# Performance work log

Hardware: AMD Instinct MI355X
Metric: run time of the kernel (lower is better)

Reference implementation:

```python
import jax, jax.numpy as jnp
import numpy as np
from jax import lax

ITER = 10
SMOOTH = 1.0


def _max_pool3(x):
    # 3x3 max pool, stride 1, pad 1 (torch pads with -inf for max pool)
    return lax.reduce_window(x, -np.inf, lax.max,
                             window_dimensions=(1, 1, 3, 3),
                             window_strides=(1, 1, 1, 1),
                             padding=((0, 0), (0, 0), (1, 1), (1, 1)))


def soft_skeletonize(x, thresh_width=ITER):
    def body(i, x):
        min_pool_x = -_max_pool3(-x)
        contour = jax.nn.relu(_max_pool3(min_pool_x) - min_pool_x)
        return jax.nn.relu(x - contour)
    return lax.fori_loop(0, thresh_width, body, x)


def setup_inputs() -> dict:
    key = jax.random.key(0)
    k1, k2 = jax.random.split(key)
    shape = (32, 2, 512, 512)
    y_pred = jax.random.uniform(k1, shape, dtype=jnp.float32)
    y_true = jax.random.uniform(k2, shape, dtype=jnp.float32)
    return {"y_pred": y_pred, "y_true": y_true}


def reference(y_pred, y_true):
    skel_pred = soft_skeletonize(y_pred, ITER)
    skel_true = soft_skeletonize(y_true, ITER)
    tprec = (jnp.sum((skel_pred * y_true)[:, 1:]) + SMOOTH) / (jnp.sum(skel_pred[:, 1:]) + SMOOTH)
    tsens = (jnp.sum((skel_true * y_pred)[:, 1:]) + SMOOTH) / (jnp.sum(skel_true[:, 1:]) + SMOOTH)
    cl_dice = 1.0 - 2.0 * (tprec * tsens) / (tprec + tsens)
    return cl_dice
```

## Files before the change

### kernel.cpp

```cpp
#include <hip/hip_runtime.h>

#define IMG 512
#define HW (IMG * IMG)
#define NB 32
#define NIMG 64
#define BAND 32
#define NBAND (IMG / BAND)
#define NSTG 5
#define HALO (2 * NSTG)
#define NROWS (BAND + 2 * HALO)
#define INF __builtin_inff()

struct Row { float4 a, b; };

static __device__ __forceinline__ float min3f(float a, float b, float c) { return fminf(fminf(a, b), c); }
static __device__ __forceinline__ float max3f(float a, float b, float c) { return fmaxf(fmaxf(a, b), c); }

static __device__ __forceinline__ Row splat(float v) {
    Row r;
    r.a = make_float4(v, v, v, v);
    r.b = make_float4(v, v, v, v);
    return r;
}

static __device__ __forceinline__ Row rmin3(const Row& x, const Row& y, const Row& z) {
    Row o;
    const float* px = (const float*)&x;
    const float* py = (const float*)&y;
    const float* pz = (const float*)&z;
    float* po = (float*)&o;
#pragma unroll
    for (int i = 0; i < 8; ++i) po[i] = min3f(px[i], py[i], pz[i]);
    return o;
}

static __device__ __forceinline__ Row rmax3(const Row& x, const Row& y, const Row& z) {
    Row o;
    const float* px = (const float*)&x;
    const float* py = (const float*)&y;
    const float* pz = (const float*)&z;
    float* po = (float*)&o;
#pragma unroll
    for (int i = 0; i < 8; ++i) po[i] = max3f(px[i], py[i], pz[i]);
    return o;
}

static __device__ __forceinline__ Row hmin3(const Row& v, int lane) {
    float shl = __shfl_up(v.b.w, 1);
    float shr = __shfl_down(v.a.x, 1);
    if (lane == 0) shl = INF;
    if (lane == 63) shr = INF;
    Row o;
    o.a.x = min3f(shl,   v.a.x, v.a.y);
    o.a.y = min3f(v.a.x, v.a.y, v.a.z);
    o.a.z = min3f(v.a.y, v.a.z, v.a.w);
    o.a.w = min3f(v.a.z, v.a.w, v.b.x);
    o.b.x = min3f(v.a.w, v.b.x, v.b.y);
    o.b.y = min3f(v.b.x, v.b.y, v.b.z);
    o.b.z = min3f(v.b.y, v.b.z, v.b.w);
    o.b.w = min3f(v.b.z, v.b.w, shr);
    return o;
}

static __device__ __forceinline__ Row hmax3(const Row& v, int lane) {
    float shl = __shfl_up(v.b.w, 1);
    float shr = __shfl_down(v.a.x, 1);
    if (lane == 0) shl = -INF;
    if (lane == 63) shr = -INF;
    Row o;
    o.a.x = max3f(shl,   v.a.x, v.a.y);
    o.a.y = max3f(v.a.x, v.a.y, v.a.z);
    o.a.z = max3f(v.a.y, v.a.z, v.a.w);
    o.a.w = max3f(v.a.z, v.a.w, v.b.x);
    o.b.x = max3f(v.a.w, v.b.x, v.b.y);
    o.b.y = max3f(v.b.x, v.b.y, v.b.z);
    o.b.z = max3f(v.b.y, v.b.z, v.b.w);
    o.b.w = max3f(v.b.z, v.b.w, shr);
    return o;
}

template <int P>
static __device__ __forceinline__ Row stage_step(Row (&x)[2], Row (&mn)[2],
                                                 const Row& xin, int t, int lane) {
    Row vmin = rmin3(x[P], x[P ^ 1], xin);
    Row mnew = hmin3(vmin, lane);
    if ((unsigned)(t - 1) >= IMG) mnew = splat(-INF);
    Row vmax = rmax3(mn[P], mn[P ^ 1], mnew);
    Row mp = hmax3(vmax, lane);
    Row out;
    {
        const float* pxc = (const float*)&x[P];
        const float* pmn = (const float*)&mn[P ^ 1];
        const float* pmp = (const float*)&mp;
        float* po = (float*)&out;
#pragma unroll
        for (int i = 0; i < 8; ++i)
            po[i] = fmaxf(pxc[i] - fmaxf(pmp[i] - pmn[i], 0.f), 0.f);
    }
    if ((unsigned)(t - 2) >= IMG) out = splat(INF);
    x[P] = xin;
    mn[P] = mnew;
    return out;
}

static __device__ __forceinline__ Row load_or_inf(const float* __restrict__ p, int r, int lane) {
    if ((unsigned)r >= IMG) return splat(INF);
    const float4* q = (const float4*)(p + (size_t)r * IMG + lane * 8);
    Row o;
    o.a = q[0];
    o.b = q[1];
    return o;
}

template <int P>
static __device__ __forceinline__ void phase_a(int r, Row (&pre)[2], Row (&x)[NSTG][2],
                                               Row (&mn)[NSTG][2], const float* __restrict__ src,
                                               float* __restrict__ dst, int B, int lane) {
    Row cur = pre[P];
    pre[P] = load_or_inf(src, r + 2, lane);
    cur = stage_step<P>(x[0], mn[0], cur, r, lane);
    cur = stage_step<P>(x[1], mn[1], cur, r - 2, lane);
    cur = stage_step<P>(x[2], mn[2], cur, r - 4, lane);
    cur = stage_step<P>(x[3], mn[3], cur, r - 6, lane);
    cur = stage_step<P>(x[4], mn[4], cur, r - 8, lane);
    const int v = r - HALO;
    if ((unsigned)(v - B) < BAND) {
        float4* q = (float4*)(dst + (size_t)v * IMG + lane * 8);
        q[0] = cur.a;
        q[1] = cur.b;
    }
}

__global__ __launch_bounds__(64, 1) void skel5_a(const float* __restrict__ yp,
                                                 const float* __restrict__ yt,
                                                 float* __restrict__ mid) {
    const int blk = blockIdx.x;
    const int img = blk >> 4, band = blk & (NBAND - 1);
    const float* src = (img < NB) ? yp + (size_t)(2 * img + 1) * HW
                                  : yt + (size_t)(2 * (img - NB) + 1) * HW;
    float* dst = mid + (size_t)img * HW;
    const int lane = threadIdx.x;
    const int B = band * BAND;

    Row x[NSTG][2], mn[NSTG][2];
#pragma unroll
    for (int j = 0; j < NSTG; ++j) {
        x[j][0] = splat(INF);  x[j][1] = splat(INF);
        mn[j][0] = splat(-INF); mn[j][1] = splat(-INF);
    }
    Row pre[2];
    pre[0] = load_or_inf(src, B - HALO, lane);
    pre[1] = load_or_inf(src, B - HALO + 1, lane);

#pragma unroll 1
    for (int rr = 0; rr < NROWS; rr += 2) {
        phase_a<0>(B - HALO + rr, pre, x, mn, src, dst, B, lane);
        phase_a<1>(B - HALO + rr + 1, pre, x, mn, src, dst, B, lane);
    }
}

template <int P>
static __device__ __forceinline__ void phase_b(int r, Row (&pre)[2], Row (&wbuf)[2],
                                               Row (&x)[NSTG][2], Row (&mn)[NSTG][2],
                                               const float* __restrict__ src,
                                               const float* __restrict__ wp, int B, int lane,
                                               float& s_prod, float& s_val) {
    Row cur = pre[P];
    pre[P] = load_or_inf(src, r + 2, lane);
    cur = stage_step<P>(x[0], mn[0], cur, r, lane);
    cur = stage_step<P>(x[1], mn[1], cur, r - 2, lane);
    cur = stage_step<P>(x[2], mn[2], cur, r - 4, lane);
    cur = stage_step<P>(x[3], mn[3], cur, r - 6, lane);
    cur = stage_step<P>(x[4], mn[4], cur, r - 8, lane);
    const int v = r - HALO;
    if ((unsigned)(v - B) < BAND) {
        const Row w = wbuf[P];
        const float* pc = (const float*)&cur;
        const float* pw = (const float*)&w;
#pragma unroll
        for (int i = 0; i < 8; ++i) {
            s_prod += pc[i] * pw[i];
            s_val += pc[i];
        }
    }
    const int vn = r + 2 - HALO;
    if ((unsigned)(vn - B) < BAND) {
        const float4* q = (const float4*)(wp + (size_t)vn * IMG + lane * 8);
        wbuf[P].a = q[0];
        wbuf[P].b = q[1];
    }
}

__global__ __launch_bounds__(64, 1) void skel5_b(const float* __restrict__ mid,
                                                 const float* __restrict__ yp,
                                                 const float* __restrict__ yt,
                                                 double* __restrict__ acc) {
    const int blk = blockIdx.x;
    const int img = blk >> 4, band = blk & (NBAND - 1);
    const float* src = mid + (size_t)img * HW;
    const float* wp = (img < NB) ? yt + (size_t)(2 * img + 1) * HW
                                 : yp + (size_t)(2 * (img - NB) + 1) * HW;
    const int lane = threadIdx.x;
    const int B = band * BAND;

    Row x[NSTG][2], mn[NSTG][2];
#pragma unroll
    for (int j = 0; j < NSTG; ++j) {
        x[j][0] = splat(INF);  x[j][1] = splat(INF);
        mn[j][0] = splat(-INF); mn[j][1] = splat(-INF);
    }
    Row pre[2], wbuf[2];
    pre[0] = load_or_inf(src, B - HALO, lane);
    pre[1] = load_or_inf(src, B - HALO + 1, lane);
    wbuf[0] = splat(0.f);
    wbuf[1] = splat(0.f);

    float s_prod = 0.f, s_val = 0.f;
#pragma unroll 1
    for (int rr = 0; rr < NROWS; rr += 2) {
        phase_b<0>(B - HALO + rr, pre, wbuf, x, mn, src, wp, B, lane, s_prod, s_val);
        phase_b<1>(B - HALO + rr + 1, pre, wbuf, x, mn, src, wp, B, lane, s_prod, s_val);
    }
#pragma unroll
    for (int off = 32; off; off >>= 1) {
        s_prod += __shfl_down(s_prod, off);
        s_val += __shfl_down(s_val, off);
    }
    if (lane == 0) {
        const int base = (img < NB) ? 0 : 2;
        atomicAdd(&acc[base], (double)s_prod);
        atomicAdd(&acc[base + 1], (double)s_val);
    }
}

__global__ void finalize(const double* __restrict__ acc, float* __restrict__ out) {
    double tprec = (acc[0] + 1.0) / (acc[1] + 1.0);
    double tsens = (acc[2] + 1.0) / (acc[3] + 1.0);
    out[0] = (float)(1.0 - 2.0 * (tprec * tsens) / (tprec + tsens));
}

extern "C" void kernel_launch(void* const* d_in, const int* in_sizes, int n_in,
                              void* d_out, int out_size, void* d_ws, size_t ws_size,
                              hipStream_t stream) {
    (void)in_sizes; (void)n_in; (void)out_size; (void)ws_size;
    const float* yp = (const float*)d_in[0];
    const float* yt = (const float*)d_in[1];
    float* out = (float*)d_out;

    float* mid = (float*)d_ws;
    double* acc = (double*)(mid + (size_t)NIMG * HW);

    hipMemsetAsync(acc, 0, 4 * sizeof(double), stream);

    const int grid = NIMG * NBAND;
    skel5_a<<<grid, 64, 0, stream>>>(yp, yt, mid);
    skel5_b<<<grid, 64, 0, stream>>>(mid, yp, yt, acc);
    finalize<<<1, 1, 0, stream>>>(acc, out);
}
```

Baseline: 275.6 us.

## Halve band height, process two rows per step, specialize edge bands

Halving the band height doubles the number of blocks, so each SIMD has more independent waves to hide latency. The pipeline step now advances two rows at once to expose more instruction-level parallelism. A template flag removes the image-boundary checks for interior bands. The cost is that the fixed halo becomes a larger share of each band, so more rows are recomputed redundantly, and the wider step raises register pressure under the new launch bound of two blocks.

```diff
diff --git a/kernel.cpp b/kernel.cpp
--- a/kernel.cpp
+++ b/kernel.cpp
@@ -4,11 +4,11 @@
 #define HW (IMG * IMG)
 #define NB 32
 #define NIMG 64
-#define BAND 32
+#define BAND 16
 #define NBAND (IMG / BAND)
 #define NSTG 5
 #define HALO (2 * NSTG)
-#define NROWS (BAND + 2 * HALO)
+#define NSTEP ((BAND + 2 * HALO) / 2)
 #define INF __builtin_inff()
 
 struct Row { float4 a, b; };
@@ -79,28 +79,44 @@
     return o;
 }
 
-template <int P>
-static __device__ __forceinline__ Row stage_step(Row (&x)[2], Row (&mn)[2],
-                                                 const Row& xin, int t, int lane) {
-    Row vmin = rmin3(x[P], x[P ^ 1], xin);
-    Row mnew = hmin3(vmin, lane);
-    if ((unsigned)(t - 1) >= IMG) mnew = splat(-INF);
-    Row vmax = rmax3(mn[P], mn[P ^ 1], mnew);
-    Row mp = hmax3(vmax, lane);
-    Row out;
+template <bool EDGE>
+static __device__ __forceinline__ void step2(Row (&x)[2], Row (&mn)[2],
+                                             Row& in0, Row& in1, int t, int lane) {
+    Row vmin0 = rmin3(x[0], x[1], in0);
+    Row vmin1 = rmin3(x[1], in0, in1);
+    Row mna = hmin3(vmin0, lane);
+    Row mnb = hmin3(vmin1, lane);
+    if (EDGE) {
+        if ((unsigned)(t - 1) >= IMG) mna = splat(-INF);
+        if ((unsigned)t >= IMG) mnb = splat(-INF);
+    }
+    Row vmax0 = rmax3(mn[0], mn[1], mna);
+    Row vmax1 = rmax3(mn[1], mna, mnb);
+    Row mp0 = hmax3(vmax0, lane);
+    Row mp1 = hmax3(vmax1, lane);
+    Row out0, out1;
     {
-        const float* pxc = (const float*)&x[P];
-        const float* pmn = (const float*)&mn[P ^ 1];
-        const float* pmp = (const float*)&mp;
-        float* po = (float*)&out;
-#pragma unroll
-        for (int i = 0; i < 8; ++i)
-            po[i] = fmaxf(pxc[i] - fmaxf(pmp[i] - pmn[i], 0.f), 0.f);
-    }
-    if ((unsigned)(t - 2) >= IMG) out = splat(INF);
-    x[P] = xin;
-    mn[P] = mnew;
-    return out;
+        const float* px0 = (const float*)&x[0];
+        const float* px1 = (const float*)&x[1];
+        const float* pm1 = (const float*)&mn[1];
+        const float* pma = (const float*)&mna;
+        const float* pp0 = (const float*)&mp0;
+        const float* pp1 = (const float*)&mp1;
+        float* po0 = (float*)&out0;
+        float* po1 = (float*)&out1;
+#pragma unroll
+        for (int i = 0; i < 8; ++i) {
+            po0[i] = fmaxf(px0[i] - fmaxf(pp0[i] - pm1[i], 0.f), 0.f);
+            po1[i] = fmaxf(px1[i] - fmaxf(pp1[i] - pma[i], 0.f), 0.f);
+        }
+    }
+    if (EDGE) {
+        if ((unsigned)(t - 2) >= IMG) out0 = splat(INF);
+        if ((unsigned)(t - 1) >= IMG) out1 = splat(INF);
+    }
+    x[0] = in0;  x[1] = in1;
+    mn[0] = mna; mn[1] = mnb;
+    in0 = out0;  in1 = out1;
 }
 
 static __device__ __forceinline__ Row load_or_inf(const float* __restrict__ p, int r, int lane) {
@@ -112,115 +128,112 @@
     return o;
 }
 
-template <int P>
-static __device__ __forceinline__ void phase_a(int r, Row (&pre)[2], Row (&x)[NSTG][2],
-                                               Row (&mn)[NSTG][2], const float* __restrict__ src,
-                                               float* __restrict__ dst, int B, int lane) {
-    Row cur = pre[P];
-    pre[P] = load_or_inf(src, r + 2, lane);
-    cur = stage_step<P>(x[0], mn[0], cur, r, lane);
-    cur = stage_step<P>(x[1], mn[1], cur, r - 2, lane);
-    cur = stage_step<P>(x[2], mn[2], cur, r - 4, lane);
-    cur = stage_step<P>(x[3], mn[3], cur, r - 6, lane);
-    cur = stage_step<P>(x[4], mn[4], cur, r - 8, lane);
-    const int v = r - HALO;
-    if ((unsigned)(v - B) < BAND) {
-        float4* q = (float4*)(dst + (size_t)v * IMG + lane * 8);
-        q[0] = cur.a;
-        q[1] = cur.b;
-    }
-}
-
-__global__ __launch_bounds__(64, 1) void skel5_a(const float* __restrict__ yp,
+template <bool EDGE>
+static __device__ __forceinline__ void run_a(const float* __restrict__ src,
+                                             float* __restrict__ dst, int B, int lane) {
+    Row x[NSTG][2], mn[NSTG][2];
+#pragma unroll
+    for (int j = 0; j < NSTG; ++j) {
+        x[j][0] = splat(INF);   x[j][1] = splat(INF);
+        mn[j][0] = splat(-INF); mn[j][1] = splat(-INF);
+    }
+    Row pre0 = load_or_inf(src, B - HALO, lane);
+    Row pre1 = load_or_inf(src, B - HALO + 1, lane);
+#pragma unroll 1
+    for (int k = 0; k < NSTEP; ++k) {
+        const int t = B - HALO + 2 * k;
+        Row in0 = pre0, in1 = pre1;
+        const int tp = (k + 1 < NSTEP) ? t + 2 : -1;
+        pre0 = load_or_inf(src, tp, lane);
+        pre1 = load_or_inf(src, tp + 1, lane);
+#pragma unroll
+        for (int j = 0; j < NSTG; ++j)
+            step2<EDGE>(x[j], mn[j], in0, in1, t - 2 * j, lane);
+        const int v = t - HALO;
+        if ((unsigned)(v - B) < BAND) {
+            float4* q0 = (float4*)(dst + (size_t)v * IMG + lane * 8);
+            q0[0] = in0.a; q0[1] = in0.b;
+            float4* q1 = (float4*)(dst + (size_t)(v + 1) * IMG + lane * 8);
+            q1[0] = in1.a; q1[1] = in1.b;
+        }
+    }
+}
+
+__global__ __launch_bounds__(64, 2) void skel5_a(const float* __restrict__ yp,
                                                  const float* __restrict__ yt,
                                                  float* __restrict__ mid) {
     const int blk = blockIdx.x;
-    const int img = blk >> 4, band = blk & (NBAND - 1);
+    const int img = blk >> 5, band = blk & (NBAND - 1);
     const float* src = (img < NB) ? yp + (size_t)(2 * img + 1) * HW
                                   : yt + (size_t)(2 * (img - NB) + 1) * HW;
     float* dst = mid + (size_t)img * HW;
     const int lane = threadIdx.x;
     const int B = band * BAND;
-
+    if (band == 0 || band == NBAND - 1) run_a<true>(src, dst, B, lane);
+    else                                run_a<false>(src, dst, B, lane);
+}
+
+template <bool EDGE>
+static __device__ __forceinline__ void run_b(const float* __restrict__ src,
+                                             const float* __restrict__ wp, int B, int lane,
+                                             float& s_prod, float& s_val) {
     Row x[NSTG][2], mn[NSTG][2];
 #pragma unroll
     for (int j = 0; j < NSTG; ++j) {
-        x[j][0] = splat(INF);  x[j][1] = splat(INF);
+        x[j][0] = splat(INF);   x[j][1] = splat(INF);
         mn[j][0] = splat(-INF); mn[j][1] = splat(-INF);
     }
-    Row pre[2];
-    pre[0] = load_or_inf(src, B - HALO, lane);
-    pre[1] = load_or_inf(src, B - HALO + 1, lane);
-
+    Row pre0 = load_or_inf(src, B - HALO, lane);
+    Row pre1 = load_or_inf(src, B - HALO + 1, lane);
 #pragma unroll 1
-    for (int rr = 0; rr < NROWS; rr += 2) {
-        phase_a<0>(B - HALO + rr, pre, x, mn, src, dst, B, lane);
-        phase_a<1>(B - HALO + rr + 1, pre, x, mn, src, dst, B, lane);
-    }
-}
-
-template <int P>
-static __device__ __forceinline__ void phase_b(int r, Row (&pre)[2], Row (&wbuf)[2],
-                                               Row (&x)[NSTG][2], Row (&mn)[NSTG][2],
-                                               const float* __restrict__ src,
-                                               const float* __restrict__ wp, int B, int lane,
-                                               float& s_prod, float& s_val) {
-    Row cur = pre[P];
-    pre[P] = load_or_inf(src, r + 2, lane);
-    cur = stage_step<P>(x[0], mn[0], cur, r, lane);
-    cur = stage_step<P>(x[1], mn[1], cur, r - 2, lane);
-    cur = stage_step<P>(x[2], mn[2], cur, r - 4, lane);
-    cur = stage_step<P>(x[3], mn[3], cur, r - 6, lane);
-    cur = stage_step<P>(x[4], mn[4], cur, r - 8, lane);
-    const int v = r - HALO;
-    if ((unsigned)(v - B) < BAND) {
-        const Row w = wbuf[P];
-        const float* pc = (const float*)&cur;
-        const float* pw = (const float*)&w;
-#pragma unroll
-        for (int i = 0; i < 8; ++i) {
-            s_prod += pc[i] * pw[i];
-            s_val += pc[i];
-        }
-    }
-    const int vn = r + 2 - HALO;
-    if ((unsigned)(vn - B) < BAND) {
-        const float4* q = (const float4*)(wp + (size_t)vn * IMG + lane * 8);
-        wbuf[P].a = q[0];
-        wbuf[P].b = q[1];
-    }
-}
-
-__global__ __launch_bounds__(64, 1) void skel5_b(const float* __restrict__ mid,
+    for (int k = 0; k < NSTEP; ++k) {
+        const int t = B - HALO + 2 * k;
+        Row in0 = pre0, in1 = pre1;
+        const int tp = (k + 1 < NSTEP) ? t + 2 : -1;
+        pre0 = load_or_inf(src, tp, lane);
+        pre1 = load_or_inf(src, tp + 1, lane);
+        const int v = t - HALO;
+        const bool inband = (unsigned)(v - B) < BAND;
+        Row w0, w1;
+        if (inband) {
+            const float4* q0 = (const float4*)(wp + (size_t)v * IMG + lane * 8);
+            w0.a = q0[0]; w0.b = q0[1];
+            const float4* q1 = (const float4*)(wp + (size_t)(v + 1) * IMG + lane * 8);
+            w1.a = q1[0]; w1.b = q1[1];
+        }
+#pragma unroll
+        for (int j = 0; j < NSTG; ++j)
+            step2<EDGE>(x[j], mn[j], in0, in1, t - 2 * j, lane);
+        if (inband) {
+            const float* p0 = (const float*)&in0;
+            const float* p1 = (const float*)&in1;
+            const float* q0 = (const float*)&w0;
+            const float* q1 = (const float*)&w1;
+#pragma unroll
+            for (int i = 0; i < 8; ++i) {
+                s_prod += p0[i] * q0[i] + p1[i] * q1[i];
+                s_val += p0[i] + p1[i];
+            }
+        }
+    }
+}
+
+__global__ __launch_bounds__(64, 2) void skel5_b(const float* __restrict__ mid,
                                                  const float* __restrict__ yp,
                                                  const float* __restrict__ yt,
                                                  double* __restrict__ acc) {
     const int blk = blockIdx.x;
-    const int img = blk >> 4, band = blk & (NBAND - 1);
+    const int img = blk >> 5, band = blk & (NBAND - 1);
     const float* src = mid + (size_t)img * HW;
     const float* wp = (img < NB) ? yt + (size_t)(2 * img + 1) * HW
                                  : yp + (size_t)(2 * (img - NB) + 1) * HW;
     const int lane = threadIdx.x;
     const int B = band * BAND;
 
-    Row x[NSTG][2], mn[NSTG][2];
-#pragma unroll
-    for (int j = 0; j < NSTG; ++j) {
-        x[j][0] = splat(INF);  x[j][1] = splat(INF);
-        mn[j][0] = splat(-INF); mn[j][1] = splat(-INF);
-    }
-    Row pre[2], wbuf[2];
-    pre[0] = load_or_inf(src, B - HALO, lane);
-    pre[1] = load_or_inf(src, B - HALO + 1, lane);
-    wbuf[0] = splat(0.f);
-    wbuf[1] = splat(0.f);
-
     float s_prod = 0.f, s_val = 0.f;
-#pragma unroll 1
-    for (int rr = 0; rr < NROWS; rr += 2) {
-        phase_b<0>(B - HALO + rr, pre, wbuf, x, mn, src, wp, B, lane, s_prod, s_val);
-        phase_b<1>(B - HALO + rr + 1, pre, wbuf, x, mn, src, wp, B, lane, s_prod, s_val);
-    }
+    if (band == 0 || band == NBAND - 1) run_b<true>(src, wp, B, lane, s_prod, s_val);
+    else                                run_b<false>(src, wp, B, lane, s_prod, s_val);
+
 #pragma unroll
     for (int off = 32; off; off >>= 1) {
         s_prod += __shfl_down(s_prod, off);
```

Result: faster. 260.0 us (-5.7%).
